# Kernel tuning notes

Hardware: AMD Instinct MI355X
Metric: run time of the kernel (lower is better)

## Reference

```python
import jax, jax.numpy as jnp
import numpy as np

NEG_INF = -1e30


def setup_inputs() -> dict:
    key = jax.random.key(0)
    k1, k2 = jax.random.split(key)
    B, S, H, D = 2, 2048, 16, 64
    qkv = jax.random.normal(k1, (B, S, 3, H, D), dtype=jnp.float32)
    pos_bias = jax.random.normal(k2, (H, S, S), dtype=jnp.float32)
    return {"qkv": qkv, "pos_bias": pos_bias}


def reference(qkv, pos_bias):
    # qkv: (B, S, 3, H, D); fixed-length path of FlashAttention.forward
    # (key_padding_mask=None, cu_seqlens=None) -> standard per-batch attention
    # with additive per-head positional bias and causal masking.
    B, S, _, H, D = qkv.shape
    q = qkv[:, :, 0]  # (B, S, H, D)
    k = qkv[:, :, 1]
    v = qkv[:, :, 2]
    softmax_scale = 1.0 / jnp.sqrt(jnp.asarray(D, dtype=qkv.dtype))
    # scores: (B, H, S, S)
    scores = jnp.einsum('bshd,bthd->bhst', q, k) * softmax_scale
    scores = scores + pos_bias[None]  # broadcast bias over batch
    # causal mask (query s attends to keys t <= s)
    causal = jnp.tril(jnp.ones((S, S), dtype=bool))
    scores = jnp.where(causal[None, None], scores, NEG_INF)
    attn = jax.nn.softmax(scores, axis=-1)
    # output: (B, S, H, D)
    out = jnp.einsum('bhst,bthd->bshd', attn, v)
    return out
```

## Files before the change

kernel.cpp:

```cpp
#include <hip/hip_runtime.h>

typedef float f32x4 __attribute__((ext_vector_type(4)));
typedef __bf16 bf16x8 __attribute__((ext_vector_type(8)));

#define MFMA16(a, b, c) __builtin_amdgcn_mfma_f32_16x16x32_bf16(a, b, c, 0, 0, 0)

constexpr int S = 2048, H = 16, Dh = 64;
constexpr int BR = 64, BC = 64;
#define NEG_INF_F (-1e30f)

__device__ __forceinline__ void gld16(const __bf16* g, __bf16* l) {
    __builtin_amdgcn_global_load_lds(
        (const __attribute__((address_space(1))) void*)(g),
        (__attribute__((address_space(3))) void*)(l), 16, 0, 0);
}

__global__ __launch_bounds__(256) void prep(const float* __restrict__ qkv,
                                            __bf16* __restrict__ khat,
                                            __bf16* __restrict__ vT)
{
    __shared__ __bf16 vtile[64][72];
    const int tid = threadIdx.x;
    const int bid = blockIdx.x;
    const int tt  = bid & 31;
    const int bh  = bid >> 5;
    const int b   = bh >> 4, h = bh & 15;
    const int t0  = tt * 64;
    const int tr  = tid >> 2, c0 = (tid & 3) * 16;

    const float* kp = qkv + (((size_t)(b * S + t0 + tr) * 3 + 1) * H + h) * Dh + c0;
    const float* vp = qkv + (((size_t)(b * S + t0 + tr) * 3 + 2) * H + h) * Dh + c0;
    f32x4 k0 = *(const f32x4*)(kp + 0), k1 = *(const f32x4*)(kp + 4),
          k2 = *(const f32x4*)(kp + 8), k3 = *(const f32x4*)(kp + 12);
    f32x4 v0 = *(const f32x4*)(vp + 0), v1 = *(const f32x4*)(vp + 4),
          v2 = *(const f32x4*)(vp + 8), v3 = *(const f32x4*)(vp + 12);
    bf16x8 ka, kb, va, vb;
#pragma unroll
    for (int j = 0; j < 4; ++j) {
        ka[j] = (__bf16)k0[j]; ka[4 + j] = (__bf16)k1[j];
        kb[j] = (__bf16)k2[j]; kb[4 + j] = (__bf16)k3[j];
        va[j] = (__bf16)v0[j]; va[4 + j] = (__bf16)v1[j];
        vb[j] = (__bf16)v2[j]; vb[4 + j] = (__bf16)v3[j];
    }
    {
        __bf16* kd = khat + ((size_t)bh * S + t0 + tr) * Dh;
        const int g0 = c0 >> 3, sw = tr & 7;
        *(bf16x8*)(kd + ((( g0    ) ^ sw) << 3)) = ka;
        *(bf16x8*)(kd + (((g0 + 1) ^ sw) << 3)) = kb;
    }
    *(bf16x8*)&vtile[tr][c0]     = va;
    *(bf16x8*)&vtile[tr][c0 + 8] = vb;
    __syncthreads();
    const int d = tid >> 2, tc0 = (tid & 3) * 16;
    bf16x8 x, y;
#pragma unroll
    for (int i = 0; i < 8; ++i) {
        x[i] = vtile[tc0 + i][d];
        y[i] = vtile[tc0 + 8 + i][d];
    }
    __bf16* vd = vT + ((size_t)bh * Dh + d) * S + t0;
    const int h0 = tc0 >> 3, sv = d & 7;
    *(bf16x8*)(vd + ((( h0    ) ^ sv) << 3)) = x;
    *(bf16x8*)(vd + (((h0 + 1) ^ sv) << 3)) = y;
}

__global__ __launch_bounds__(256, 4) void fa_fwd(
    const float* __restrict__ qkv, const float* __restrict__ pb,
    const __bf16* __restrict__ khat, const __bf16* __restrict__ vT,
    float* __restrict__ out)
{
    __shared__ __bf16 klds[64 * 64];
    __shared__ __bf16 vlds[64 * 64];
    __shared__ __bf16 plds[4][16][72];

    const int tid  = threadIdx.x;
    const int wave = tid >> 6;
    const int lane = tid & 63;
    const int quad = lane >> 4;
    const int l16  = lane & 15;

    const int g  = blockIdx.x >> 8;
    const int pp = blockIdx.x & 255;
    const int kk = pp >> 5, hb = pp & 31;
    const int b  = hb & 1, h = hb >> 1;
    const int qt = (g == 0) ? 31 - kk : (g == 1) ? 16 + kk : (g == 2) ? 15 - kk : kk;
    const int q0 = qt * BR;
    const int bh = b * H + h;
    const float scale = 0.125f;

    const int qrow = q0 + wave * 16 + l16;
    const float* qp = qkv + (((size_t)(b * S + qrow) * 3 + 0) * H + h) * Dh;
    bf16x8 qfrag[2];
#pragma unroll
    for (int ks = 0; ks < 2; ++ks) {
        f32x4 a = *(const f32x4*)(qp + ks * 32 + quad * 8);
        f32x4 c = *(const f32x4*)(qp + ks * 32 + quad * 8 + 4);
#pragma unroll
        for (int j = 0; j < 4; ++j) qfrag[ks][j] = (__bf16)a[j];
#pragma unroll
        for (int j = 0; j < 4; ++j) qfrag[ks][4 + j] = (__bf16)c[j];
    }

    const int lrow  = wave * 16 + quad * 4;
    const int myrow = q0 + lrow;
    float l_r[4] = {0.f, 0.f, 0.f, 0.f};
    f32x4 oacc[4];
#pragma unroll
    for (int dt = 0; dt < 4; ++dt) oacc[dt] = (f32x4){0.f, 0.f, 0.f, 0.f};

    const int seg = wave * 2;
    const int lt  = lane >> 3, le = (lane & 7) * 8;
    const __bf16* kg = khat + ((size_t)bh * S + (seg * 8 + lt)) * 64 + le;
    const __bf16* vg = vT   + ((size_t)bh * Dh + seg * 8 + lt) * S + le;
    __bf16* kl = klds + seg * 512;
    __bf16* vl = vlds + seg * 512;

    const float* bb = pb + (size_t)h * S * S + (size_t)myrow * S + l16;
    const int swz = l16 & 7;

    for (int it = 0; it <= qt; ++it) {
        __syncthreads();
        gld16(kg,         kl);
        gld16(kg + 512,   kl + 512);
        gld16(vg,         vl);
        gld16(vg + 8 * S, vl + 512);
        kg += BC * 64; vg += BC;

        float breg[16];
#pragma unroll
        for (int ct = 0; ct < 4; ++ct)
#pragma unroll
            for (int r = 0; r < 4; ++r) breg[ct * 4 + r] = bb[(size_t)r * S + ct * 16];
        bb += BC;
        __syncthreads();

        f32x4 sacc[4];
#pragma unroll
        for (int ct = 0; ct < 4; ++ct) sacc[ct] = (f32x4){0.f, 0.f, 0.f, 0.f};
#pragma unroll
        for (int ct = 0; ct < 4; ++ct) {
#pragma unroll
            for (int ks = 0; ks < 2; ++ks) {
                bf16x8 kf = *(const bf16x8*)&klds[(ct * 16 + l16) * 64 + (((ks * 4 + quad) ^ swz) << 3)];
                sacc[ct] = MFMA16(qfrag[ks], kf, sacc[ct]);
            }
        }

        const bool diag = (it == qt);
#pragma unroll
        for (int ct = 0; ct < 4; ++ct) {
            const int colrel = ct * 16 + l16;
#pragma unroll
            for (int r = 0; r < 4; ++r) {
                float s = fmaf(sacc[ct][r], scale, breg[ct * 4 + r]);
                if (diag && (colrel > lrow + r)) s = NEG_INF_F;
                float p = __expf(s);
                l_r[r] += p;
                plds[wave][quad * 4 + r][colrel] = (__bf16)p;
            }
        }

        bf16x8 pf[2];
#pragma unroll
        for (int ks = 0; ks < 2; ++ks)
            pf[ks] = *(const bf16x8*)&plds[wave][l16][ks * 32 + quad * 8];
#pragma unroll
        for (int dt = 0; dt < 4; ++dt) {
#pragma unroll
            for (int ks = 0; ks < 2; ++ks) {
                bf16x8 vf = *(const bf16x8*)&vlds[(dt * 16 + l16) * 64 + (((ks * 4 + quad) ^ swz) << 3)];
                oacc[dt] = MFMA16(pf[ks], vf, oacc[dt]);
            }
        }
    }

#pragma unroll
    for (int r = 0; r < 4; ++r) {
#pragma unroll
        for (int m = 1; m < 16; m <<= 1) l_r[r] += __shfl_xor(l_r[r], m, 64);
        const float inv = 1.0f / l_r[r];
        float* op = out + (((size_t)(b * S + (myrow + r)) * H) + h) * Dh;
#pragma unroll
        for (int dt = 0; dt < 4; ++dt)
            op[dt * 16 + l16] = oacc[dt][r] * inv;
    }
}

extern "C" void kernel_launch(void* const* d_in, const int* in_sizes, int n_in,
                              void* d_out, int out_size, void* d_ws, size_t ws_size,
                              hipStream_t stream) {
    const float* qkv = (const float*)d_in[0];
    const float* pb  = (const float*)d_in[1];
    float* out       = (float*)d_out;

    constexpr size_t KV_ELEMS = (size_t)2 * H * S * Dh;
    __bf16* khat = (__bf16*)d_ws;
    __bf16* vT   = khat + KV_ELEMS;

    prep<<<dim3(1024), dim3(256), 0, stream>>>(qkv, khat, vT);
    fa_fwd<<<dim3(1024), dim3(256), 0, stream>>>(qkv, pb, khat, vT, out);
}
```

Before: 398.2 us.

## Software-pipeline K/V and bias loads with double-buffered V tile

Moves the next tile's K/V global-to-LDS loads and positional-bias register loads so they are issued during the current tile's softmax and PV MFMA work, instead of stalling at the start of each iteration. V is double-buffered in LDS, and K reuses its single buffer after a barrier that follows QK^T. MFMA sections are wrapped in s_setprio to favour matrix issue across waves. This adds LDS use (8 KB more) and register pressure from prefetched bias values, which may reduce occupancy at launch bounds of 4 blocks. Whether the barriers are placed correctly for the async V loads is not obvious, since the reads of vlds[cur] at iteration it+1 are not visibly waited on.

```diff
diff --git a/kernel.cpp b/kernel.cpp
--- a/kernel.cpp
+++ b/kernel.cpp
@@ -70,7 +70,7 @@
     float* __restrict__ out)
 {
     __shared__ __bf16 klds[64 * 64];
-    __shared__ __bf16 vlds[64 * 64];
+    __shared__ __bf16 vlds[2][64 * 64];
     __shared__ __bf16 plds[4][16][72];
 
     const int tid  = threadIdx.x;
@@ -113,30 +113,32 @@
     const __bf16* kg = khat + ((size_t)bh * S + (seg * 8 + lt)) * 64 + le;
     const __bf16* vg = vT   + ((size_t)bh * Dh + seg * 8 + lt) * S + le;
     __bf16* kl = klds + seg * 512;
-    __bf16* vl = vlds + seg * 512;
+    const int vo = seg * 512;
 
     const float* bb = pb + (size_t)h * S * S + (size_t)myrow * S + l16;
     const int swz = l16 & 7;
 
+    gld16(kg,         kl);
+    gld16(kg + 512,   kl + 512);
+    gld16(vg,         vlds[0] + vo);
+    gld16(vg + 8 * S, vlds[0] + vo + 512);
+    kg += BC * 64; vg += BC;
+
+    float bnext[16];
+#pragma unroll
+    for (int ct = 0; ct < 4; ++ct)
+#pragma unroll
+        for (int r = 0; r < 4; ++r) bnext[ct * 4 + r] = bb[(size_t)r * S + ct * 16];
+    bb += BC;
+
     for (int it = 0; it <= qt; ++it) {
+        const int cur = it & 1;
         __syncthreads();
-        gld16(kg,         kl);
-        gld16(kg + 512,   kl + 512);
-        gld16(vg,         vl);
-        gld16(vg + 8 * S, vl + 512);
-        kg += BC * 64; vg += BC;
-
-        float breg[16];
-#pragma unroll
-        for (int ct = 0; ct < 4; ++ct)
-#pragma unroll
-            for (int r = 0; r < 4; ++r) breg[ct * 4 + r] = bb[(size_t)r * S + ct * 16];
-        bb += BC;
-        __syncthreads();
 
         f32x4 sacc[4];
 #pragma unroll
         for (int ct = 0; ct < 4; ++ct) sacc[ct] = (f32x4){0.f, 0.f, 0.f, 0.f};
+        __builtin_amdgcn_s_setprio(1);
 #pragma unroll
         for (int ct = 0; ct < 4; ++ct) {
 #pragma unroll
@@ -145,6 +147,18 @@
                 sacc[ct] = MFMA16(qfrag[ks], kf, sacc[ct]);
             }
         }
+        __builtin_amdgcn_s_setprio(0);
+
+        __syncthreads();
+
+        if (it < qt) {
+            gld16(kg,         kl);
+            gld16(kg + 512,   kl + 512);
+            __bf16* vl = &vlds[cur ^ 1][vo];
+            gld16(vg,         vl);
+            gld16(vg + 8 * S, vl + 512);
+            kg += BC * 64; vg += BC;
+        }
 
         const bool diag = (it == qt);
 #pragma unroll
@@ -152,26 +166,34 @@
             const int colrel = ct * 16 + l16;
 #pragma unroll
             for (int r = 0; r < 4; ++r) {
-                float s = fmaf(sacc[ct][r], scale, breg[ct * 4 + r]);
+                float s = fmaf(sacc[ct][r], scale, bnext[ct * 4 + r]);
                 if (diag && (colrel > lrow + r)) s = NEG_INF_F;
                 float p = __expf(s);
                 l_r[r] += p;
                 plds[wave][quad * 4 + r][colrel] = (__bf16)p;
             }
-        }
+            if (it < qt) {
+#pragma unroll
+                for (int r = 0; r < 4; ++r)
+                    bnext[ct * 4 + r] = bb[(size_t)r * S + ct * 16];
+            }
+        }
+        if (it < qt) bb += BC;
 
         bf16x8 pf[2];
 #pragma unroll
         for (int ks = 0; ks < 2; ++ks)
             pf[ks] = *(const bf16x8*)&plds[wave][l16][ks * 32 + quad * 8];
+        __builtin_amdgcn_s_setprio(1);
 #pragma unroll
         for (int dt = 0; dt < 4; ++dt) {
 #pragma unroll
             for (int ks = 0; ks < 2; ++ks) {
-                bf16x8 vf = *(const bf16x8*)&vlds[(dt * 16 + l16) * 64 + (((ks * 4 + quad) ^ swz) << 3)];
+                bf16x8 vf = *(const bf16x8*)&vlds[cur][(dt * 16 + l16) * 64 + (((ks * 4 + quad) ^ swz) << 3)];
                 oacc[dt] = MFMA16(pf[ks], vf, oacc[dt]);
             }
         }
+        __builtin_amdgcn_s_setprio(0);
     }
 
 #pragma unroll
```

Measured after the change: 399.1 us. Within noise of the previous version (+0.2%).
